# Optimization experiments

Hardware: AMD Instinct MI355X
Metric: run time of the kernel (lower is better)

The kernel has to match this reference:

```python
import jax, jax.numpy as jnp
import numpy as np

B, T, H, L = 2048, 128, 48, 3  # batch, n_weights (= seq steps), hidden_dim, n_layers


def setup_inputs() -> dict:
    key = jax.random.key(0)
    ks = jax.random.split(key, 9)
    s = 0.05
    adj = jax.random.bernoulli(ks[0], 0.5, (B, T)).astype(jnp.float32)  # 0/1 adjacency entries
    eps = jax.random.normal(ks[1], (B, T), jnp.float32)  # standard-normal noise for rsample
    Wi = jax.random.normal(ks[2], (H, 1), jnp.float32) * s   # embed_input: Linear(1, H)
    bi = jnp.zeros((H,), jnp.float32)
    Wa = jax.random.normal(ks[3], (H, T), jnp.float32) * s   # embed_adj: Linear(n_weights, H)
    ba = jnp.zeros((H,), jnp.float32)
    Wp = jax.random.normal(ks[4], (1, H), jnp.float32) * s   # proj_mean: Linear(H, 1)
    bp = jnp.zeros((1,), jnp.float32)
    Wih = jax.random.normal(ks[5], (L, 4 * H, H), jnp.float32) * s  # LSTM input weights per layer
    Whh = jax.random.normal(ks[6], (L, 4 * H, H), jnp.float32) * s  # LSTM hidden weights per layer
    bih = jnp.zeros((L, 4 * H), jnp.float32)
    bhh = jnp.zeros((L, 4 * H), jnp.float32)
    h0 = 0.001 * jax.random.normal(ks[7], (L, H), jnp.float32)  # learned initial hidden state
    c0 = 0.001 * jax.random.normal(ks[8], (L, H), jnp.float32)  # learned initial cell state
    return dict(adj=adj, eps=eps, Wi=Wi, bi=bi, Wa=Wa, ba=ba, Wp=Wp, bp=bp,
                Wih=Wih, Whh=Whh, bih=bih, bhh=bhh, h0=h0, c0=c0)


def _lstm_cell(x, h, c, Wih_l, Whh_l, bih_l, bhh_l):
    # PyTorch LSTMCell math, gate order i, f, g, o
    gates = x @ Wih_l.T + bih_l + h @ Whh_l.T + bhh_l  # [B, 4H]
    i, f, g, o = jnp.split(gates, 4, axis=-1)
    c_new = jax.nn.sigmoid(f) * c + jax.nn.sigmoid(i) * jnp.tanh(g)
    h_new = jax.nn.sigmoid(o) * jnp.tanh(c_new)
    return h_new, c_new


def reference(adj, eps, Wi, bi, Wa, ba, Wp, bp, Wih, Whh, bih, bhh, h0, c0):
    n = adj.shape[0]
    # embed_adj(adj): constant across steps (the torch code recomputes it every step; same value)
    adj_emb = adj @ Wa.T + ba  # [B, H]
    h = jnp.broadcast_to(h0[:, None, :], (L, n, H))
    c = jnp.broadcast_to(c0[:, None, :], (L, n, H))
    inp0 = jnp.zeros((n, 1), adj.dtype)  # _init_input_param is a zeros parameter

    def step(carry, xs):
        h, c, inp = carry
        eps_t, adj_t = xs  # each [B]
        x = (inp @ Wi.T + bi) * adj_emb  # embed_input(inp) * embed_adj(adj), [B, H]
        hs, cs = [], []
        for l in range(L):  # 3 stacked LSTM layers, seq_len 1 per step
            x, c_l = _lstm_cell(x, h[l], c[l], Wih[l], Whh[l], bih[l], bhh[l])
            hs.append(x)
            cs.append(c_l)
        mean = x @ Wp.T + bp  # proj_mean, [B, 1]; std is fixed at 1
        # reparameterized sample from Normal(mean, 1), masked by adjacency column t
        sample = (mean[:, 0] + eps_t) * adj_t  # [B]
        return (jnp.stack(hs), jnp.stack(cs), sample[:, None]), sample

    _, samples = jax.lax.scan(step, (h, c, inp0), (eps.T, adj.T))
    return samples.T  # [B, n_weights]
```

## Files before the change

kernel.cpp:

```cpp
#include <hip/hip_runtime.h>
#include <hip/hip_bf16.h>


using bf16x8 = __attribute__((ext_vector_type(8))) __bf16;
using u16x8  = __attribute__((ext_vector_type(8))) unsigned short;
using f32x4  = __attribute__((ext_vector_type(4))) float;
using f32x2  = __attribute__((ext_vector_type(2))) float;

__device__ __forceinline__ float fexp2(float x){ return __builtin_amdgcn_exp2f(x); }
__device__ __forceinline__ float frcp (float x){ return __builtin_amdgcn_rcpf(x); }
__device__ __forceinline__ float sigm (float x){ return frcp(1.f + fexp2(-1.44269504f*x)); }
__device__ __forceinline__ float tanha(float x){ return 1.f - 2.f*frcp(1.f + fexp2(2.88539008f*x)); }

__device__ __forceinline__ unsigned short f2bf(float x){
  unsigned u = __float_as_uint(x);
  return (unsigned short)((u + 0x7FFFu + ((u>>16)&1u)) >> 16);
}

__device__ __forceinline__ f32x4 mfma16(u16x8 a, u16x8 b, f32x4 c){
  return __builtin_amdgcn_mfma_f32_16x16x32_bf16(
      __builtin_bit_cast(bf16x8, a), __builtin_bit_cast(bf16x8, b), c, 0, 0, 0);
}

__device__ __forceinline__ void cell_update(
    const f32x4& ac0, const f32x4& ac1, const f32x4& ac2, const f32x4& ac3,
    bool lo, float& cv0, float& cv1, float& hv0, float& hv1)
{
  const float gi0 = lo ? ac0[0] : ac0[2], gi1 = lo ? ac0[1] : ac0[3];
  const float gf0 = lo ? ac1[0] : ac1[2], gf1 = lo ? ac1[1] : ac1[3];
  const float gg0 = lo ? ac2[0] : ac2[2], gg1 = lo ? ac2[1] : ac2[3];
  const float go0 = lo ? ac3[0] : ac3[2], go1 = lo ? ac3[1] : ac3[3];
  const float cn0 = sigm(gf0)*cv0 + sigm(gi0)*tanha(gg0);
  const float cn1 = sigm(gf1)*cv1 + sigm(gi1)*tanha(gg1);
  cv0 = cn0; cv1 = cn1;
  hv0 = sigm(go0)*tanha(cn0);
  hv1 = sigm(go1)*tanha(cn1);
}

#define MM4(A, WK) \
  ac0 = mfma16(A, WK[0], ac0); ac1 = mfma16(A, WK[1], ac1); \
  ac2 = mfma16(A, WK[2], ac2); ac3 = mfma16(A, WK[3], ac3);

__global__ __launch_bounds__(192, 1) void lstm_fused(
    const float* __restrict__ adj, const float* __restrict__ eps,
    const float* __restrict__ Wi,  const float* __restrict__ bi,
    const float* __restrict__ Wa,  const float* __restrict__ ba,
    const float* __restrict__ Wp,  const float* __restrict__ bp,
    const float* __restrict__ Wih, const float* __restrict__ Whh,
    const float* __restrict__ bih, const float* __restrict__ bhh,
    const float* __restrict__ h0,  const float* __restrict__ c0,
    float* __restrict__ out)
{
  const int tid   = threadIdx.x;
  const int wv    = tid >> 6;
  const int lane  = tid & 63;
  const int c     = lane & 15;
  const int kg    = lane >> 4;
  const int j     = 16*wv + c;
  const int b0    = blockIdx.x * 8;
  const int bq    = 4*(kg & 1);
  const int bbase = bq + 2*(kg >> 1);
  const bool lo   = (kg < 2);

  __shared__ __align__(16) unsigned short hbuf[3][8][104];
  __shared__ __align__(16) float adjT[128][8];
  __shared__ __align__(16) float epsT[128][8];
  __shared__ __align__(16) float partial[3][8];

  u16x8 wf1[3][4], wf2[3][4];
  u16x8 wf0[2][4], wfx[2][4];
  float biasr1[4], biasr2[4], biasr0[4];
#pragma unroll
  for (int kk = 0; kk < 3; ++kk) {
    const int k0 = 32*kk + 8*kg;
#pragma unroll
    for (int g = 0; g < 4; ++g) {
      const int n = 48*g + j;
#pragma unroll
      for (int l = 1; l < 3; ++l) {
        const float* src = (k0 < 48) ? (Wih + ((l*192 + n)*48 + k0))
                                     : (Whh + ((l*192 + n)*48 + (k0 - 48)));
        float4 p0 = *reinterpret_cast<const float4*>(src);
        float4 p1 = *reinterpret_cast<const float4*>(src + 4);
        u16x8 f;
        f[0]=f2bf(p0.x); f[1]=f2bf(p0.y); f[2]=f2bf(p0.z); f[3]=f2bf(p0.w);
        f[4]=f2bf(p1.x); f[5]=f2bf(p1.y); f[6]=f2bf(p1.z); f[7]=f2bf(p1.w);
        if (l == 1) wf1[kk][g] = f; else wf2[kk][g] = f;
      }
    }
  }
#pragma unroll
  for (int kk = 0; kk < 2; ++kk) {
    const int k0 = 32*kk + 8*kg;
#pragma unroll
    for (int g = 0; g < 4; ++g) {
      const int n = 48*g + j;
      u16x8 fh = {0,0,0,0,0,0,0,0}, fx = fh;
      if (k0 < 48) {
        const float* sh = Whh + (n*48 + k0);
        const float* sx = Wih + (n*48 + k0);
        float4 p0 = *reinterpret_cast<const float4*>(sh);
        float4 p1 = *reinterpret_cast<const float4*>(sh + 4);
        fh[0]=f2bf(p0.x); fh[1]=f2bf(p0.y); fh[2]=f2bf(p0.z); fh[3]=f2bf(p0.w);
        fh[4]=f2bf(p1.x); fh[5]=f2bf(p1.y); fh[6]=f2bf(p1.z); fh[7]=f2bf(p1.w);
        p0 = *reinterpret_cast<const float4*>(sx);
        p1 = *reinterpret_cast<const float4*>(sx + 4);
        fx[0]=f2bf(p0.x); fx[1]=f2bf(p0.y); fx[2]=f2bf(p0.z); fx[3]=f2bf(p0.w);
        fx[4]=f2bf(p1.x); fx[5]=f2bf(p1.y); fx[6]=f2bf(p1.z); fx[7]=f2bf(p1.w);
      }
      wf0[kk][g] = fh; wfx[kk][g] = fx;
    }
  }
#pragma unroll
  for (int g = 0; g < 4; ++g) {
    const int n = 48*g + j;
    biasr0[g] = bih[        n] + bhh[        n];
    biasr1[g] = bih[192   + n] + bhh[192   + n];
    biasr2[g] = bih[2*192 + n] + bhh[2*192 + n];
  }

  for (int i = tid; i < 256; i += 192) {
    const int b = i >> 5, q = i & 31;
    const float4 va = reinterpret_cast<const float4*>(adj + (size_t)(b0+b)*128)[q];
    adjT[4*q+0][b]=va.x; adjT[4*q+1][b]=va.y; adjT[4*q+2][b]=va.z; adjT[4*q+3][b]=va.w;
    const float4 ve = reinterpret_cast<const float4*>(eps + (size_t)(b0+b)*128)[q];
    epsT[4*q+0][b]=ve.x; epsT[4*q+1][b]=ve.y; epsT[4*q+2][b]=ve.z; epsT[4*q+3][b]=ve.w;
  }
  const float Wp_j = Wp[j];
  const float bp0  = bp[0];
  __syncthreads();

  for (int cid = tid; cid < 384; cid += 192) {
    const int b = cid & 7, jj = cid >> 3;
    float s = ba[jj];
    const float* wr = Wa + jj*128;
    for (int t2 = 0; t2 < 128; ++t2) s += adjT[t2][b] * wr[t2];
    hbuf[0][b][jj] = f2bf(Wi[jj] * s);
    hbuf[1][b][jj] = f2bf(bi[jj] * s);
  }
  for (int cid = tid; cid < 384; cid += 192) {
    const int l = cid / 128, r2 = cid % 128, b = r2 >> 4, jj = 48 + (r2 & 15);
    hbuf[l][b][jj] = 0;
  }
  __syncthreads();

  f32x4 uu[4], vb0[4];
  {
    const f32x4 z4 = {0.f,0.f,0.f,0.f};
    const unsigned short* rp = &hbuf[0][c & 7][0];
    u16x8 A0 = *reinterpret_cast<const u16x8*>(rp + 8*kg);
    u16x8 A1 = *reinterpret_cast<const u16x8*>(rp + 32 + 8*kg);
#pragma unroll
    for (int g = 0; g < 4; ++g)
      uu[g] = mfma16(A1, wfx[1][g], mfma16(A0, wfx[0][g], z4));
    rp = &hbuf[1][c & 7][0];
    A0 = *reinterpret_cast<const u16x8*>(rp + 8*kg);
    A1 = *reinterpret_cast<const u16x8*>(rp + 32 + 8*kg);
#pragma unroll
    for (int g = 0; g < 4; ++g) {
      f32x4 v = mfma16(A1, wfx[1][g], mfma16(A0, wfx[0][g], z4));
      const f32x4 bsp = {biasr0[g], biasr0[g], biasr0[g], biasr0[g]};
      vb0[g] = v + bsp;
    }
  }
  __syncthreads();

  for (int cid = tid; cid < 1152; cid += 192) {
    const int l = cid / 384, r2 = cid % 384, b = r2 & 7, jj = r2 >> 3;
    hbuf[l][b][jj] = f2bf(h0[l*48 + jj]);
  }
  float cc00, cc01, cc10, cc11, cc20, cc21;
  cc00 = cc01 = c0[       j];
  cc10 = cc11 = c0[48   + j];
  cc20 = cc21 = c0[2*48 + j];
  __syncthreads();

  u16x8 a00 = *reinterpret_cast<const u16x8*>(&hbuf[0][c & 7][8*kg]);
  u16x8 a01 = *reinterpret_cast<const u16x8*>(&hbuf[0][c & 7][32 + 8*kg]);

  f32x4 sampv = {0.f,0.f,0.f,0.f};
  const f32x4 bp4 = {bp0, bp0, bp0, bp0};

  for (int t = 0; t < 128; ++t) {
    if (t > 0) {
      const f32x4 q0 = *reinterpret_cast<const f32x4*>(&partial[0][bq]);
      const f32x4 q1 = *reinterpret_cast<const f32x4*>(&partial[1][bq]);
      const f32x4 q2 = *reinterpret_cast<const f32x4*>(&partial[2][bq]);
      const f32x4 pe = *reinterpret_cast<const f32x4*>(&epsT[t-1][bq]);
      const f32x4 pa = *reinterpret_cast<const f32x4*>(&adjT[t-1][bq]);
      sampv = (q0 + q1 + q2 + bp4 + pe) * pa;
      if (wv == 0 && c == 0) {
        const float sA = lo ? sampv[0] : sampv[2];
        const float sB = lo ? sampv[1] : sampv[3];
        out[(size_t)(b0 + bbase    )*128 + (t-1)] = sA;
        out[(size_t)(b0 + bbase + 1)*128 + (t-1)] = sB;
      }
    }
    f32x4 ac0 = vb0[0] + sampv*uu[0];
    f32x4 ac1 = vb0[1] + sampv*uu[1];
    f32x4 ac2 = vb0[2] + sampv*uu[2];
    f32x4 ac3 = vb0[3] + sampv*uu[3];
    MM4(a00, wf0[0]);
    MM4(a01, wf0[1]);
    u16x8 a11 = {0,0,0,0,0,0,0,0}, a12;
    if (kg >= 2) a11 = *reinterpret_cast<const u16x8*>(&hbuf[1][c & 7][8*kg - 16]);
    a12 = *reinterpret_cast<const u16x8*>(&hbuf[1][c & 7][16 + 8*kg]);
    {
      float hv0, hv1;
      cell_update(ac0, ac1, ac2, ac3, lo, cc00, cc01, hv0, hv1);
      hbuf[0][bbase    ][j] = f2bf(hv0);
      hbuf[0][bbase + 1][j] = f2bf(hv1);
    }
    __syncthreads();
    {
      const unsigned short* rp = &hbuf[0][c & 7][0];
      const u16x8 a10 = *reinterpret_cast<const u16x8*>(rp + 8*kg);
      if (kg < 2) a11 = *reinterpret_cast<const u16x8*>(rp + 32 + 8*kg);
      ac0 = (f32x4){biasr1[0], biasr1[0], biasr1[0], biasr1[0]};
      ac1 = (f32x4){biasr1[1], biasr1[1], biasr1[1], biasr1[1]};
      ac2 = (f32x4){biasr1[2], biasr1[2], biasr1[2], biasr1[2]};
      ac3 = (f32x4){biasr1[3], biasr1[3], biasr1[3], biasr1[3]};
      MM4(a10, wf1[0]);
      MM4(a11, wf1[1]);
      MM4(a12, wf1[2]);
    }
    u16x8 a21 = {0,0,0,0,0,0,0,0}, a22;
    if (kg >= 2) a21 = *reinterpret_cast<const u16x8*>(&hbuf[2][c & 7][8*kg - 16]);
    a22 = *reinterpret_cast<const u16x8*>(&hbuf[2][c & 7][16 + 8*kg]);
    {
      float hv0, hv1;
      cell_update(ac0, ac1, ac2, ac3, lo, cc10, cc11, hv0, hv1);
      hbuf[1][bbase    ][j] = f2bf(hv0);
      hbuf[1][bbase + 1][j] = f2bf(hv1);
    }
    __syncthreads();
    {
      const unsigned short* rp = &hbuf[1][c & 7][0];
      const u16x8 a20 = *reinterpret_cast<const u16x8*>(rp + 8*kg);
      if (kg < 2) a21 = *reinterpret_cast<const u16x8*>(rp + 32 + 8*kg);
      ac0 = (f32x4){biasr2[0], biasr2[0], biasr2[0], biasr2[0]};
      ac1 = (f32x4){biasr2[1], biasr2[1], biasr2[1], biasr2[1]};
      ac2 = (f32x4){biasr2[2], biasr2[2], biasr2[2], biasr2[2]};
      ac3 = (f32x4){biasr2[3], biasr2[3], biasr2[3], biasr2[3]};
      MM4(a20, wf2[0]);
      MM4(a21, wf2[1]);
      MM4(a22, wf2[2]);
    }
    a00 = *reinterpret_cast<const u16x8*>(&hbuf[0][c & 7][8*kg]);
    a01 = *reinterpret_cast<const u16x8*>(&hbuf[0][c & 7][32 + 8*kg]);
    float hp0, hp1;
    cell_update(ac0, ac1, ac2, ac3, lo, cc20, cc21, hp0, hp1);
    hbuf[2][bbase    ][j] = f2bf(hp0);
    hbuf[2][bbase + 1][j] = f2bf(hp1);
    float pr0 = hp0 * Wp_j, pr1 = hp1 * Wp_j;
#pragma unroll
    for (int m = 1; m < 16; m <<= 1) {
      pr0 += __shfl_xor(pr0, m, 64);
      pr1 += __shfl_xor(pr1, m, 64);
    }
    if (c == 0) {
      f32x2 v = {pr0, pr1};
      *reinterpret_cast<f32x2*>(&partial[wv][bbase]) = v;
    }
    __syncthreads();
  }
  {
    const f32x4 q0 = *reinterpret_cast<const f32x4*>(&partial[0][bq]);
    const f32x4 q1 = *reinterpret_cast<const f32x4*>(&partial[1][bq]);
    const f32x4 q2 = *reinterpret_cast<const f32x4*>(&partial[2][bq]);
    const f32x4 pe = *reinterpret_cast<const f32x4*>(&epsT[127][bq]);
    const f32x4 pa = *reinterpret_cast<const f32x4*>(&adjT[127][bq]);
    const f32x4 sv = (q0 + q1 + q2 + bp4 + pe) * pa;
    if (wv == 0 && c == 0) {
      const float sA = lo ? sv[0] : sv[2];
      const float sB = lo ? sv[1] : sv[3];
      out[(size_t)(b0 + bbase    )*128 + 127] = sA;
      out[(size_t)(b0 + bbase + 1)*128 + 127] = sB;
    }
  }
}

extern "C" void kernel_launch(void* const* d_in, const int* in_sizes, int n_in,
                              void* d_out, int out_size, void* d_ws, size_t ws_size,
                              hipStream_t stream) {
  const float* adj = (const float*)d_in[0];
  const float* eps = (const float*)d_in[1];
  const float* Wi  = (const float*)d_in[2];
  const float* bi  = (const float*)d_in[3];
  const float* Wa  = (const float*)d_in[4];
  const float* ba  = (const float*)d_in[5];
  const float* Wp  = (const float*)d_in[6];
  const float* bp  = (const float*)d_in[7];
  const float* Wih = (const float*)d_in[8];
  const float* Whh = (const float*)d_in[9];
  const float* bih = (const float*)d_in[10];
  const float* bhh = (const float*)d_in[11];
  const float* h0  = (const float*)d_in[12];
  const float* c0  = (const float*)d_in[13];

  lstm_fused<<<dim3(2048/8), dim3(192), 0, stream>>>(
      adj, eps, Wi, bi, Wa, ba, Wp, bp, Wih, Whh, bih, bhh, h0, c0, (float*)d_out);
}
```

Baseline: 175.0 us.

## Compute projection via MFMA, prefetch layer-0 recurrent matmul, buffer outputs in LDS

The output projection is now computed redundantly in every wave with two MFMAs over the layer-2 hidden state. This replaces the shuffle reduction and the cross-wave partial sums in shared memory. The h-dependent part of the layer-0 gates is now computed at the end of the previous step, overlapping it with layer 2 and shortening the critical path at the start of each step. Samples are staged in an LDS buffer and written to global memory coalesced at the end, and hidden states are packed to bf16 with a single conversion instruction. The trade-off is extra MFMA work and more registers per wave.

```diff
diff --git a/kernel.cpp b/kernel.cpp
--- a/kernel.cpp
+++ b/kernel.cpp
@@ -5,7 +5,6 @@
 using bf16x8 = __attribute__((ext_vector_type(8))) __bf16;
 using u16x8  = __attribute__((ext_vector_type(8))) unsigned short;
 using f32x4  = __attribute__((ext_vector_type(4))) float;
-using f32x2  = __attribute__((ext_vector_type(2))) float;
 
 __device__ __forceinline__ float fexp2(float x){ return __builtin_amdgcn_exp2f(x); }
 __device__ __forceinline__ float frcp (float x){ return __builtin_amdgcn_rcpf(x); }
@@ -22,9 +21,9 @@
       __builtin_bit_cast(bf16x8, a), __builtin_bit_cast(bf16x8, b), c, 0, 0, 0);
 }
 
-__device__ __forceinline__ void cell_update(
+__device__ __forceinline__ unsigned cell2(
     const f32x4& ac0, const f32x4& ac1, const f32x4& ac2, const f32x4& ac3,
-    bool lo, float& cv0, float& cv1, float& hv0, float& hv1)
+    bool lo, float& cv0, float& cv1)
 {
   const float gi0 = lo ? ac0[0] : ac0[2], gi1 = lo ? ac0[1] : ac0[3];
   const float gf0 = lo ? ac1[0] : ac1[2], gf1 = lo ? ac1[1] : ac1[3];
@@ -33,8 +32,11 @@
   const float cn0 = sigm(gf0)*cv0 + sigm(gi0)*tanha(gg0);
   const float cn1 = sigm(gf1)*cv1 + sigm(gi1)*tanha(gg1);
   cv0 = cn0; cv1 = cn1;
-  hv0 = sigm(go0)*tanha(cn0);
-  hv1 = sigm(go1)*tanha(cn1);
+  const float hv0 = sigm(go0)*tanha(cn0);
+  const float hv1 = sigm(go1)*tanha(cn1);
+  unsigned pk;
+  asm("v_cvt_pk_bf16_f32 %0, %1, %2" : "=v"(pk) : "v"(hv0), "v"(hv1));
+  return pk;
 }
 
 #define MM4(A, WK) \
@@ -65,10 +67,11 @@
   __shared__ __align__(16) unsigned short hbuf[3][8][104];
   __shared__ __align__(16) float adjT[128][8];
   __shared__ __align__(16) float epsT[128][8];
-  __shared__ __align__(16) float partial[3][8];
+  __shared__ __align__(16) float outb[128][8];
 
   u16x8 wf1[3][4], wf2[3][4];
   u16x8 wf0[2][4], wfx[2][4];
+  u16x8 wpf[2];
   float biasr1[4], biasr2[4], biasr0[4];
 #pragma unroll
   for (int kk = 0; kk < 3; ++kk) {
@@ -110,6 +113,13 @@
       }
       wf0[kk][g] = fh; wfx[kk][g] = fx;
     }
+    u16x8 fp = {0,0,0,0,0,0,0,0};
+#pragma unroll
+    for (int e = 0; e < 8; ++e) {
+      const int k = k0 + e;
+      if (k < 48) fp[e] = f2bf(Wp[k]);
+    }
+    wpf[kk] = fp;
   }
 #pragma unroll
   for (int g = 0; g < 4; ++g) {
@@ -126,8 +136,7 @@
     const float4 ve = reinterpret_cast<const float4*>(eps + (size_t)(b0+b)*128)[q];
     epsT[4*q+0][b]=ve.x; epsT[4*q+1][b]=ve.y; epsT[4*q+2][b]=ve.z; epsT[4*q+3][b]=ve.w;
   }
-  const float Wp_j = Wp[j];
-  const float bp0  = bp[0];
+  const float bp0 = bp[0];
   __syncthreads();
 
   for (int cid = tid; cid < 384; cid += 192) {
@@ -175,108 +184,104 @@
   cc20 = cc21 = c0[2*48 + j];
   __syncthreads();
 
-  u16x8 a00 = *reinterpret_cast<const u16x8*>(&hbuf[0][c & 7][8*kg]);
-  u16x8 a01 = *reinterpret_cast<const u16x8*>(&hbuf[0][c & 7][32 + 8*kg]);
-
+  f32x4 g0, g1, g2, g3;
+  {
+    const unsigned short* rp = &hbuf[0][c & 7][0];
+    const u16x8 A0 = *reinterpret_cast<const u16x8*>(rp + 8*kg);
+    const u16x8 A1 = *reinterpret_cast<const u16x8*>(rp + 32 + 8*kg);
+    g0 = vb0[0]; g1 = vb0[1]; g2 = vb0[2]; g3 = vb0[3];
+    g0 = mfma16(A0, wf0[0][0], g0); g1 = mfma16(A0, wf0[0][1], g1);
+    g2 = mfma16(A0, wf0[0][2], g2); g3 = mfma16(A0, wf0[0][3], g3);
+    g0 = mfma16(A1, wf0[1][0], g0); g1 = mfma16(A1, wf0[1][1], g1);
+    g2 = mfma16(A1, wf0[1][2], g2); g3 = mfma16(A1, wf0[1][3], g3);
+  }
+
+  const f32x4 bp4 = {bp0, bp0, bp0, bp0};
   f32x4 sampv = {0.f,0.f,0.f,0.f};
-  const f32x4 bp4 = {bp0, bp0, bp0, bp0};
 
   for (int t = 0; t < 128; ++t) {
-    if (t > 0) {
-      const f32x4 q0 = *reinterpret_cast<const f32x4*>(&partial[0][bq]);
-      const f32x4 q1 = *reinterpret_cast<const f32x4*>(&partial[1][bq]);
-      const f32x4 q2 = *reinterpret_cast<const f32x4*>(&partial[2][bq]);
-      const f32x4 pe = *reinterpret_cast<const f32x4*>(&epsT[t-1][bq]);
-      const f32x4 pa = *reinterpret_cast<const f32x4*>(&adjT[t-1][bq]);
-      sampv = (q0 + q1 + q2 + bp4 + pe) * pa;
-      if (wv == 0 && c == 0) {
-        const float sA = lo ? sampv[0] : sampv[2];
-        const float sB = lo ? sampv[1] : sampv[3];
-        out[(size_t)(b0 + bbase    )*128 + (t-1)] = sA;
-        out[(size_t)(b0 + bbase + 1)*128 + (t-1)] = sB;
-      }
-    }
-    f32x4 ac0 = vb0[0] + sampv*uu[0];
-    f32x4 ac1 = vb0[1] + sampv*uu[1];
-    f32x4 ac2 = vb0[2] + sampv*uu[2];
-    f32x4 ac3 = vb0[3] + sampv*uu[3];
-    MM4(a00, wf0[0]);
-    MM4(a01, wf0[1]);
+    if (t) {
+      const u16x8 mh0 = *reinterpret_cast<const u16x8*>(&hbuf[2][c & 7][8*kg]);
+      const u16x8 mh1 = *reinterpret_cast<const u16x8*>(&hbuf[2][c & 7][32 + 8*kg]);
+      const f32x4 ev = *reinterpret_cast<const f32x4*>(&epsT[t-1][bq]);
+      const f32x4 av = *reinterpret_cast<const f32x4*>(&adjT[t-1][bq]);
+      f32x4 mz = {0.f,0.f,0.f,0.f};
+      mz = mfma16(mh0, wpf[0], mz);
+      mz = mfma16(mh1, wpf[1], mz);
+      sampv = (mz + bp4 + ev) * av;
+      if (tid == 0 || tid == 16)
+        *reinterpret_cast<f32x4*>(&outb[t-1][bq]) = sampv;
+    }
+    g0 += sampv*uu[0]; g1 += sampv*uu[1]; g2 += sampv*uu[2]; g3 += sampv*uu[3];
+    {
+      const unsigned pk = cell2(g0, g1, g2, g3, lo, cc00, cc01);
+      hbuf[0][bbase    ][j] = (unsigned short)pk;
+      hbuf[0][bbase + 1][j] = (unsigned short)(pk >> 16);
+    }
     u16x8 a11 = {0,0,0,0,0,0,0,0}, a12;
     if (kg >= 2) a11 = *reinterpret_cast<const u16x8*>(&hbuf[1][c & 7][8*kg - 16]);
     a12 = *reinterpret_cast<const u16x8*>(&hbuf[1][c & 7][16 + 8*kg]);
-    {
-      float hv0, hv1;
-      cell_update(ac0, ac1, ac2, ac3, lo, cc00, cc01, hv0, hv1);
-      hbuf[0][bbase    ][j] = f2bf(hv0);
-      hbuf[0][bbase + 1][j] = f2bf(hv1);
-    }
     __syncthreads();
     {
       const unsigned short* rp = &hbuf[0][c & 7][0];
       const u16x8 a10 = *reinterpret_cast<const u16x8*>(rp + 8*kg);
       if (kg < 2) a11 = *reinterpret_cast<const u16x8*>(rp + 32 + 8*kg);
-      ac0 = (f32x4){biasr1[0], biasr1[0], biasr1[0], biasr1[0]};
-      ac1 = (f32x4){biasr1[1], biasr1[1], biasr1[1], biasr1[1]};
-      ac2 = (f32x4){biasr1[2], biasr1[2], biasr1[2], biasr1[2]};
-      ac3 = (f32x4){biasr1[3], biasr1[3], biasr1[3], biasr1[3]};
+      f32x4 ac0 = {biasr1[0], biasr1[0], biasr1[0], biasr1[0]};
+      f32x4 ac1 = {biasr1[1], biasr1[1], biasr1[1], biasr1[1]};
+      f32x4 ac2 = {biasr1[2], biasr1[2], biasr1[2], biasr1[2]};
+      f32x4 ac3 = {biasr1[3], biasr1[3], biasr1[3], biasr1[3]};
+      MM4(a12, wf1[2]);
       MM4(a10, wf1[0]);
       MM4(a11, wf1[1]);
-      MM4(a12, wf1[2]);
+      const unsigned pk = cell2(ac0, ac1, ac2, ac3, lo, cc10, cc11);
+      hbuf[1][bbase    ][j] = (unsigned short)pk;
+      hbuf[1][bbase + 1][j] = (unsigned short)(pk >> 16);
     }
     u16x8 a21 = {0,0,0,0,0,0,0,0}, a22;
     if (kg >= 2) a21 = *reinterpret_cast<const u16x8*>(&hbuf[2][c & 7][8*kg - 16]);
     a22 = *reinterpret_cast<const u16x8*>(&hbuf[2][c & 7][16 + 8*kg]);
-    {
-      float hv0, hv1;
-      cell_update(ac0, ac1, ac2, ac3, lo, cc10, cc11, hv0, hv1);
-      hbuf[1][bbase    ][j] = f2bf(hv0);
-      hbuf[1][bbase + 1][j] = f2bf(hv1);
-    }
     __syncthreads();
     {
       const unsigned short* rp = &hbuf[1][c & 7][0];
       const u16x8 a20 = *reinterpret_cast<const u16x8*>(rp + 8*kg);
       if (kg < 2) a21 = *reinterpret_cast<const u16x8*>(rp + 32 + 8*kg);
-      ac0 = (f32x4){biasr2[0], biasr2[0], biasr2[0], biasr2[0]};
-      ac1 = (f32x4){biasr2[1], biasr2[1], biasr2[1], biasr2[1]};
-      ac2 = (f32x4){biasr2[2], biasr2[2], biasr2[2], biasr2[2]};
-      ac3 = (f32x4){biasr2[3], biasr2[3], biasr2[3], biasr2[3]};
+      const unsigned short* rp0 = &hbuf[0][c & 7][0];
+      const u16x8 a00 = *reinterpret_cast<const u16x8*>(rp0 + 8*kg);
+      const u16x8 a01 = *reinterpret_cast<const u16x8*>(rp0 + 32 + 8*kg);
+      f32x4 ac0 = {biasr2[0], biasr2[0], biasr2[0], biasr2[0]};
+      f32x4 ac1 = {biasr2[1], biasr2[1], biasr2[1], biasr2[1]};
+      f32x4 ac2 = {biasr2[2], biasr2[2], biasr2[2], biasr2[2]};
+      f32x4 ac3 = {biasr2[3], biasr2[3], biasr2[3], biasr2[3]};
+      MM4(a22, wf2[2]);
       MM4(a20, wf2[0]);
       MM4(a21, wf2[1]);
-      MM4(a22, wf2[2]);
-    }
-    a00 = *reinterpret_cast<const u16x8*>(&hbuf[0][c & 7][8*kg]);
-    a01 = *reinterpret_cast<const u16x8*>(&hbuf[0][c & 7][32 + 8*kg]);
-    float hp0, hp1;
-    cell_update(ac0, ac1, ac2, ac3, lo, cc20, cc21, hp0, hp1);
-    hbuf[2][bbase    ][j] = f2bf(hp0);
-    hbuf[2][bbase + 1][j] = f2bf(hp1);
-    float pr0 = hp0 * Wp_j, pr1 = hp1 * Wp_j;
-#pragma unroll
-    for (int m = 1; m < 16; m <<= 1) {
-      pr0 += __shfl_xor(pr0, m, 64);
-      pr1 += __shfl_xor(pr1, m, 64);
-    }
-    if (c == 0) {
-      f32x2 v = {pr0, pr1};
-      *reinterpret_cast<f32x2*>(&partial[wv][bbase]) = v;
+      const unsigned pk = cell2(ac0, ac1, ac2, ac3, lo, cc20, cc21);
+      hbuf[2][bbase    ][j] = (unsigned short)pk;
+      hbuf[2][bbase + 1][j] = (unsigned short)(pk >> 16);
+      g0 = vb0[0]; g1 = vb0[1]; g2 = vb0[2]; g3 = vb0[3];
+      g0 = mfma16(a00, wf0[0][0], g0); g1 = mfma16(a00, wf0[0][1], g1);
+      g2 = mfma16(a00, wf0[0][2], g2); g3 = mfma16(a00, wf0[0][3], g3);
+      g0 = mfma16(a01, wf0[1][0], g0); g1 = mfma16(a01, wf0[1][1], g1);
+      g2 = mfma16(a01, wf0[1][2], g2); g3 = mfma16(a01, wf0[1][3], g3);
     }
     __syncthreads();
   }
   {
-    const f32x4 q0 = *reinterpret_cast<const f32x4*>(&partial[0][bq]);
-    const f32x4 q1 = *reinterpret_cast<const f32x4*>(&partial[1][bq]);
-    const f32x4 q2 = *reinterpret_cast<const f32x4*>(&partial[2][bq]);
-    const f32x4 pe = *reinterpret_cast<const f32x4*>(&epsT[127][bq]);
-    const f32x4 pa = *reinterpret_cast<const f32x4*>(&adjT[127][bq]);
-    const f32x4 sv = (q0 + q1 + q2 + bp4 + pe) * pa;
-    if (wv == 0 && c == 0) {
-      const float sA = lo ? sv[0] : sv[2];
-      const float sB = lo ? sv[1] : sv[3];
-      out[(size_t)(b0 + bbase    )*128 + 127] = sA;
-      out[(size_t)(b0 + bbase + 1)*128 + 127] = sB;
-    }
+    const u16x8 mh0 = *reinterpret_cast<const u16x8*>(&hbuf[2][c & 7][8*kg]);
+    const u16x8 mh1 = *reinterpret_cast<const u16x8*>(&hbuf[2][c & 7][32 + 8*kg]);
+    const f32x4 ev = *reinterpret_cast<const f32x4*>(&epsT[127][bq]);
+    const f32x4 av = *reinterpret_cast<const f32x4*>(&adjT[127][bq]);
+    f32x4 mz = {0.f,0.f,0.f,0.f};
+    mz = mfma16(mh0, wpf[0], mz);
+    mz = mfma16(mh1, wpf[1], mz);
+    const f32x4 sv = (mz + bp4 + ev) * av;
+    if (tid == 0 || tid == 16)
+      *reinterpret_cast<f32x4*>(&outb[127][bq]) = sv;
+  }
+  __syncthreads();
+  for (int i = tid; i < 1024; i += 192) {
+    const int b = i >> 7, tt = i & 127;
+    out[(size_t)(b0 + b)*128 + tt] = outb[tt][b];
   }
 }
 
```

New measurement: 150.5 us, median of 4. 14.0% less time.
